# Performance work log

Hardware: AMD Instinct MI355X
Metric: run time of the kernel (lower is better)

## Reference

```python
import jax, jax.numpy as jnp
import numpy as np

N, E, D_IN, HID, OUT, H = 50000, 800000, 64, 128, 128, 8


def _lin(key, fan_in, fan_out, bias=True):
    k1, k2 = jax.random.split(key)
    W = jax.random.normal(k1, (fan_in, fan_out), jnp.float32) / np.sqrt(fan_in)
    if bias:
        b = jax.random.normal(k2, (fan_out,), jnp.float32) * 0.01
        return W, b
    return (W,)


def setup_inputs() -> dict:
    key = jax.random.key(0)
    ks = jax.random.split(key, 40)
    inp = {
        "x": jax.random.normal(ks[0], (N, D_IN), jnp.float32),
        "edge_index": jax.random.randint(ks[1], (2, E), 0, N, jnp.int64),
        "edge_attr": jax.random.normal(ks[2], (E, D_IN), jnp.float32),
    }
    dims = [(D_IN, HID), (HID, HID), (HID, OUT)]  # (in, heads*out_ch) per layer
    ki = 3
    for l, (di, do) in enumerate(dims):
        inp[f"Wq{l}"], inp[f"bq{l}"] = _lin(ks[ki], di, do); ki += 1
        inp[f"Wk{l}"], inp[f"bk{l}"] = _lin(ks[ki], di, do); ki += 1
        inp[f"Wv{l}"], inp[f"bv{l}"] = _lin(ks[ki], di, do); ki += 1
        (inp[f"We{l}"],) = _lin(ks[ki], D_IN, do, bias=False); ki += 1
        inp[f"Ws{l}"], inp[f"bs{l}"] = _lin(ks[ki], di, do); ki += 1
    for l in range(2):
        inp[f"g{l}"] = jnp.ones((HID,), jnp.float32)
        inp[f"be{l}"] = jnp.zeros((HID,), jnp.float32)
    return inp


def _transformer_conv(x, src, dst, edge_attr, Wq, bq, Wk, bk, Wv, bv, We, Ws, bs):
    n = x.shape[0]
    hc = Wq.shape[1]
    c = hc // H
    q = (x @ Wq + bq).reshape(n, H, c)
    k = (x @ Wk + bk).reshape(n, H, c)
    v = (x @ Wv + bv).reshape(n, H, c)
    e = (edge_attr @ We).reshape(-1, H, c)  # [E,H,c]
    ke = k[src] + e                          # edge-wise key + edge proj
    alpha = jnp.einsum("ehc,ehc->eh", q[dst], ke) / jnp.sqrt(jnp.float32(c))
    m = jax.ops.segment_max(alpha, dst, num_segments=n)
    m = jnp.where(jnp.isfinite(m), m, 0.0)
    p = jnp.exp(alpha - m[dst])
    s = jax.ops.segment_sum(p, dst, num_segments=n)
    a = p / (s[dst] + 1e-16)                 # segment softmax over in-edges
    msg = (v[src] + e) * a[..., None]
    out = jax.ops.segment_sum(msg, dst, num_segments=n).reshape(n, hc)
    return out + x @ Ws + bs                 # root/skip connection


def _bn(x, g, b):
    mu = jnp.mean(x, axis=0)
    var = jnp.mean(jnp.square(x - mu), axis=0)
    return g * (x - mu) * jax.lax.rsqrt(var + 1e-5) + b


def reference(x, edge_index, edge_attr,
              Wq0, bq0, Wk0, bk0, Wv0, bv0, We0, Ws0, bs0,
              Wq1, bq1, Wk1, bk1, Wv1, bv1, We1, Ws1, bs1,
              Wq2, bq2, Wk2, bk2, Wv2, bv2, We2, Ws2, bs2,
              g0, be0, g1, be1):
    src, dst = edge_index[0], edge_index[1]
    h = _transformer_conv(x, src, dst, edge_attr, Wq0, bq0, Wk0, bk0, Wv0, bv0, We0, Ws0, bs0)
    h = jax.nn.relu(_bn(h, g0, be0))
    h = _transformer_conv(h, src, dst, edge_attr, Wq1, bq1, Wk1, bk1, Wv1, bv1, We1, Ws1, bs1)
    h = jax.nn.relu(_bn(h, g1, be1))
    h = _transformer_conv(h, src, dst, edge_attr, Wq2, bq2, Wk2, bk2, Wv2, bv2, We2, Ws2, bs2)
    return h, edge_attr
```

## Files before the change

### kernel.cpp

```cpp
#include <hip/hip_runtime.h>
#include <hip/hip_bf16.h>

typedef __attribute__((ext_vector_type(8))) short short8;
typedef __attribute__((ext_vector_type(4))) float f32x4;
typedef unsigned short ushort_t;
typedef __attribute__((ext_vector_type(2))) unsigned short ushort2v;
typedef __attribute__((ext_vector_type(2))) unsigned int uint2v;
typedef __attribute__((ext_vector_type(4))) unsigned int uint4v;

static __device__ __forceinline__ ushort_t f2bf(float x) {
    __hip_bfloat16 h = __float2bfloat16(x);
    return *(ushort_t*)&h;
}
static __device__ __forceinline__ float bflo(unsigned int u) { return __uint_as_float(u << 16); }
static __device__ __forceinline__ float bfhi(unsigned int u) { return __uint_as_float(u & 0xffff0000u); }
static __device__ __forceinline__ float bfu(ushort_t u) { return __uint_as_float((unsigned int)u << 16); }

template <int CTRL>
static __device__ __forceinline__ float dpp_xadd(float x) {
    int y = __builtin_amdgcn_update_dpp(0, __float_as_int(x), CTRL, 0xF, 0xF, true);
    return x + __int_as_float(y);
}


__global__ void hist_kernel(const int* __restrict__ dst, int E, int* __restrict__ hist) {
    int i = blockIdx.x * blockDim.x + threadIdx.x;
    if (i < E) atomicAdd(&hist[dst[i]], 1);
}

__global__ __launch_bounds__(1024) void scan_block_kernel(
    const int* __restrict__ hist, int n, int* __restrict__ row_ptr, int* __restrict__ bsums)
{
    __shared__ int lds[1024];
    int tid = threadIdx.x;
    int i = blockIdx.x * 1024 + tid;
    int vv = (i < n) ? hist[i] : 0;
    lds[tid] = vv;
    __syncthreads();
    for (int off = 1; off < 1024; off <<= 1) {
        int t = (tid >= off) ? lds[tid - off] : 0;
        __syncthreads();
        lds[tid] += t;
        __syncthreads();
    }
    if (i < n) row_ptr[i] = lds[tid] - vv;
    if (tid == 1023) bsums[blockIdx.x] = lds[1023];
}

__global__ void scan_tops_kernel(int* __restrict__ bsums, int nb) {
    if (threadIdx.x == 0 && blockIdx.x == 0) {
        int run = 0;
        for (int i = 0; i < nb; i++) { int t = bsums[i]; bsums[i] = run; run += t; }
    }
}

__global__ __launch_bounds__(256) void scan_add_kernel(
    const int* __restrict__ bsums, int n, int total,
    int* __restrict__ row_ptr, int* __restrict__ cursor)
{
    int i = blockIdx.x * blockDim.x + threadIdx.x;
    if (i < n) {
        int vv = row_ptr[i] + bsums[i >> 10];
        row_ptr[i] = vv;
        cursor[i] = vv;
    }
    if (i == 0) row_ptr[n] = total;
}

__global__ void scatter_kernel(const int* __restrict__ src, const int* __restrict__ dst, int E,
                               int* __restrict__ cursor, int* __restrict__ eid, int* __restrict__ srcs) {
    int i = blockIdx.x * blockDim.x + threadIdx.x;
    if (i < E) {
        int d = dst[i];
        int pos = atomicAdd(&cursor[d], 1);
        eid[pos] = i;
        srcs[pos] = src[i];
    }
}

__global__ __launch_bounds__(256) void permute_ea_kernel(
    const float* __restrict__ edge_attr, const int* __restrict__ eid, int E,
    ushort_t* __restrict__ ea)
{
    int idx = blockIdx.x * blockDim.x + threadIdx.x;
    if (idx >= E * 8) return;
    int j = idx >> 3, seg = idx & 7;
    int rsrc = eid[j];
    const float* s = edge_attr + (size_t)rsrc * 64 + seg * 8;
    float4 f0 = *(const float4*)s;
    float4 f1 = *(const float4*)(s + 4);
    short8 o;
    o[0] = f2bf(f0.x); o[1] = f2bf(f0.y); o[2] = f2bf(f0.z); o[3] = f2bf(f0.w);
    o[4] = f2bf(f1.x); o[5] = f2bf(f1.y); o[6] = f2bf(f1.z); o[7] = f2bf(f1.w);
    *(short8*)(ea + (size_t)j * 64 + seg * 8) = o;
}

__global__ __launch_bounds__(256) void pack_Wnode_kernel(
    const float* __restrict__ Wq, const float* __restrict__ Wk,
    const float* __restrict__ Wv, const float* __restrict__ Ws,
    int DI, ushort_t* __restrict__ dst)
{
    int NKF = DI >> 5;
    int total = DI * 512;
    int idx = blockIdx.x * blockDim.x + threadIdx.x;
    if (idx >= total) return;
    int j = idx & 7;
    int lane = (idx >> 3) & 63;
    int rest = idx >> 9;
    int kf = rest % NKF;
    int t = rest / NKF;
    int kdim = kf * 32 + (lane >> 4) * 8 + j;
    int ncol = t * 16 + (lane & 15);
    const float* W = (ncol < 128) ? Wq : (ncol < 256) ? Wk : (ncol < 384) ? Wv : Ws;
    dst[idx] = f2bf(W[kdim * 128 + (ncol & 127)]);
}

__global__ __launch_bounds__(256) void pack_bias_kernel(
    const float* __restrict__ bq, const float* __restrict__ bk,
    const float* __restrict__ bv, const float* __restrict__ bs,
    float* __restrict__ dst)
{
    int i = threadIdx.x + blockIdx.x * blockDim.x;
    if (i >= 512) return;
    const float* b = (i < 128) ? bq : (i < 256) ? bk : (i < 384) ? bv : bs;
    dst[i] = b[i & 127];
}

__global__ __launch_bounds__(256) void pack_We_kernel(
    const float* __restrict__ We0, const float* __restrict__ We1,
    const float* __restrict__ We2, ushort_t* __restrict__ Bpack)
{
    int idx = blockIdx.x * blockDim.x + threadIdx.x;
    if (idx >= 3 * 8192) return;
    int j = idx & 7;
    int lane = (idx >> 3) & 63;
    int kk = (idx >> 9) & 1;
    int t = (idx >> 10) & 7;
    int layer = idx >> 13;
    const float* We = (layer == 0) ? We0 : (layer == 1) ? We1 : We2;
    int kdim = kk * 32 + (lane >> 4) * 8 + j;
    int ncol = t * 16 + (lane & 15);
    Bpack[idx] = f2bf(We[kdim * 128 + ncol]);
}

template <int DI, bool BN>
__global__ __launch_bounds__(256) void node_gemm_mfma_kernel(
    const float* __restrict__ hin, int N,
    const ushort_t* __restrict__ Bpack, const float* __restrict__ biasc,
    const float* __restrict__ scale, const float* __restrict__ shift,
    float* __restrict__ qout, unsigned int* __restrict__ kvout,
    float* __restrict__ skipout)
{
    constexpr int NKF = DI / 32;
    __shared__ float ctile[64][132];
    __shared__ ushort_t ctileK[64][136];
    int wave = threadIdx.x >> 6;
    int lane = threadIdx.x & 63;
    int tid = threadIdx.x;
    int base = blockIdx.x * 64;
    int m0 = base + wave * 16;

    int mrow = min(m0 + (lane & 15), N - 1);
    const float* arow = hin + (size_t)mrow * DI;
    int koff = (lane >> 4) * 8;

    short8 a[NKF];
#pragma unroll
    for (int kf = 0; kf < NKF; kf++) {
        float4 fa = *(const float4*)(arow + kf * 32 + koff);
        float4 fb = *(const float4*)(arow + kf * 32 + koff + 4);
        if constexpr (BN) {
            int c0 = kf * 32 + koff;
            float4 sa = *(const float4*)(scale + c0);
            float4 sb = *(const float4*)(scale + c0 + 4);
            float4 ha = *(const float4*)(shift + c0);
            float4 hb = *(const float4*)(shift + c0 + 4);
            fa.x = fmaxf(fa.x * sa.x + ha.x, 0.f);
            fa.y = fmaxf(fa.y * sa.y + ha.y, 0.f);
            fa.z = fmaxf(fa.z * sa.z + ha.z, 0.f);
            fa.w = fmaxf(fa.w * sa.w + ha.w, 0.f);
            fb.x = fmaxf(fb.x * sb.x + hb.x, 0.f);
            fb.y = fmaxf(fb.y * sb.y + hb.y, 0.f);
            fb.z = fmaxf(fb.z * sb.z + hb.z, 0.f);
            fb.w = fmaxf(fb.w * sb.w + hb.w, 0.f);
        }
        short8 t;
        t[0] = f2bf(fa.x); t[1] = f2bf(fa.y); t[2] = f2bf(fa.z); t[3] = f2bf(fa.w);
        t[4] = f2bf(fb.x); t[5] = f2bf(fb.y); t[6] = f2bf(fb.z); t[7] = f2bf(fb.w);
        a[kf] = t;
    }

    const short8* Bp = (const short8*)Bpack;
    f32x4 acc[32];
#pragma unroll
    for (int t = 0; t < 32; t++) acc[t] = (f32x4){0.f, 0.f, 0.f, 0.f};
#pragma unroll
    for (int t = 0; t < 32; t++) {
#pragma unroll
        for (int kf = 0; kf < NKF; kf++)
            acc[t] = __builtin_amdgcn_mfma_f32_16x16x32_bf16(a[kf], Bp[(t * NKF + kf) * 64 + lane], acc[t], 0, 0, 0);
    }

    int crow = (lane >> 4) * 4;
    int ccol = lane & 15;

#pragma unroll
    for (int t8 = 0; t8 < 8; t8++) {
        float bb = biasc[t8 * 16 + ccol];
#pragma unroll
        for (int r = 0; r < 4; r++)
            ctile[wave * 16 + crow + r][t8 * 16 + ccol] = acc[t8][r] + bb;
    }
    __syncthreads();
#pragma unroll
    for (int it = 0; it < 8; it++) {
        int idx4 = it * 256 + tid;
        int row = idx4 >> 5;
        int c4 = idx4 & 31;
        int gr = base + row;
        if (gr < N)
            *(float4*)(qout + (size_t)gr * 128 + c4 * 4) = *(const float4*)&ctile[row][c4 * 4];
    }
    __syncthreads();

#pragma unroll
    for (int t8 = 0; t8 < 8; t8++) {
        float bb = biasc[128 + t8 * 16 + ccol];
#pragma unroll
        for (int r = 0; r < 4; r++)
            ctileK[wave * 16 + crow + r][t8 * 16 + ccol] = f2bf(acc[8 + t8][r] + bb);
    }
#pragma unroll
    for (int t8 = 0; t8 < 8; t8++) {
        float bb = biasc[256 + t8 * 16 + ccol];
#pragma unroll
        for (int r = 0; r < 4; r++)
            ctile[wave * 16 + crow + r][t8 * 16 + ccol] = acc[16 + t8][r] + bb;
    }
    __syncthreads();
#pragma unroll
    for (int it = 0; it < 4; it++) {
        int idx8 = it * 256 + tid;
        int row = idx8 >> 4;
        int c8 = idx8 & 15;
        int gr = base + row;
        if (gr < N) {
            const float* vs = &ctile[row][c8 * 8];
            uint4v o0, o1;
#pragma unroll
            for (int i = 0; i < 4; i++) {
                ushort2v kp2 = *(const ushort2v*)&ctileK[row][c8 * 8 + 2 * i];
                unsigned int kp = (unsigned int)kp2[0] | ((unsigned int)kp2[1] << 16);
                unsigned int vp = (unsigned int)f2bf(vs[2 * i]) | ((unsigned int)f2bf(vs[2 * i + 1]) << 16);
                if (i < 2) { o0[2 * i] = kp; o0[2 * i + 1] = vp; }
                else       { o1[2 * (i - 2)] = kp; o1[2 * (i - 2) + 1] = vp; }
            }
            unsigned int* dp = kvout + (size_t)gr * 128 + c8 * 8;
            *(uint4v*)dp = o0;
            *(uint4v*)(dp + 4) = o1;
        }
    }
    __syncthreads();

#pragma unroll
    for (int t8 = 0; t8 < 8; t8++) {
        float bb = biasc[384 + t8 * 16 + ccol];
#pragma unroll
        for (int r = 0; r < 4; r++)
            ctile[wave * 16 + crow + r][t8 * 16 + ccol] = acc[24 + t8][r] + bb;
    }
    __syncthreads();
#pragma unroll
    for (int it = 0; it < 8; it++) {
        int idx4 = it * 256 + tid;
        int row = idx4 >> 5;
        int c4 = idx4 & 31;
        int gr = base + row;
        if (gr < N)
            *(float4*)(skipout + (size_t)gr * 128 + c4 * 4) = *(const float4*)&ctile[row][c4 * 4];
    }
}

#define PROCESS8(B)                                                              \
    {                                                                            \
        ushort2v eev[8];                                                         \
        float p[8];                                                              \
        _Pragma("unroll")                                                        \
        for (int u = 0; u < 8; u++)                                              \
            eev[u] = *(const ushort2v*)&elds[wave][(B) * 8 + u][2 * lane];       \
        _Pragma("unroll")                                                        \
        for (int u = 0; u < 8; u++) {                                            \
            uint2v kvp = kvr[(B) * 8 + u];                                       \
            p[u] = qq.x * (bflo(kvp[0]) + bfu(eev[u][0]))                        \
                 + qq.y * (bfhi(kvp[0]) + bfu(eev[u][1]));                       \
        }                                                                        \
        _Pragma("unroll")                                                        \
        for (int u = 0; u < 8; u++) {                                            \
            p[u] = dpp_xadd<0xB1>(p[u]);                                         \
            p[u] = dpp_xadd<0x4E>(p[u]);                                         \
            p[u] = dpp_xadd<0x141>(p[u]);       \
        }                                                                        \
        _Pragma("unroll")                                                        \
        for (int u = 0; u < 8; u++) {                                            \
            float wv = __expf(p[u] * 0.25f);                                     \
            if (c0 + (B) * 8 + u >= je) wv = 0.f;                                \
            uint2v kvp = kvr[(B) * 8 + u];                                       \
            acc0 += wv * (bflo(kvp[1]) + bfu(eev[u][0]));                        \
            acc1 += wv * (bfhi(kvp[1]) + bfu(eev[u][1]));                        \
            sw += wv;                                                            \
        }                                                                        \
    }

__global__ __launch_bounds__(256) void agg_fused_kernel(
    const int* __restrict__ row_ptr, const int* __restrict__ srcs,
    const float* __restrict__ q, const unsigned int* __restrict__ kvbuf,
    const ushort_t* __restrict__ ea, const ushort_t* __restrict__ BpackWe,
    float* __restrict__ hout, int N)
{
    __shared__ ushort_t elds[4][16][136];
    int tid = threadIdx.x;
    int wave = tid >> 6, lane = tid & 63;
    int n = blockIdx.x * 4 + wave;
    if (n >= N) return;

    const short8* BpG = (const short8*)BpackWe;
    short8 bq[16];
#pragma unroll
    for (int i = 0; i < 16; i++) bq[i] = BpG[i * 64 + lane];

    const float2* q2 = (const float2*)q;
    float2* h2 = (float2*)hout;

    int ch = lane & 15, kg = lane >> 4;
    float2 qq = q2[(size_t)n * 64 + lane];
    float2 sk = h2[(size_t)n * 64 + lane];
    float acc0 = 0.f, acc1 = 0.f, sw = 0.f;
    int jb = row_ptr[n], je = row_ptr[n + 1];

    short8 a0 = {}, a1 = {};
    int sv = 0;
    if (jb < je) {
        int j0 = min(jb + ch, je - 1);
        sv = srcs[j0];
        const ushort_t* row0 = ea + (size_t)j0 * 64;
        a0 = *(const short8*)(row0 + kg * 8);
        a1 = *(const short8*)(row0 + 32 + kg * 8);
    }

    for (int c0 = jb; c0 < je; c0 += 16) {
        uint2v kvr[16];
#pragma unroll
        for (int u = 0; u < 16; u++) {
            int su = __builtin_amdgcn_readlane(sv, u);
            kvr[u] = *(const uint2v*)(kvbuf + (size_t)su * 128 + 2 * lane);
        }

#pragma unroll
        for (int t = 0; t < 8; t++) {
            f32x4 z = (f32x4){0.f, 0.f, 0.f, 0.f};
            z = __builtin_amdgcn_mfma_f32_16x16x32_bf16(a0, bq[t * 2 + 0], z, 0, 0, 0);
            z = __builtin_amdgcn_mfma_f32_16x16x32_bf16(a1, bq[t * 2 + 1], z, 0, 0, 0);
#pragma unroll
            for (int r = 0; r < 4; r++)
                elds[wave][kg * 4 + r][t * 16 + ch] = f2bf(z[r]);
        }

        int cn = c0 + 16;
        short8 na0 = a0, na1 = a1;
        int nsv = sv;
        if (cn < je) {
            int jn = min(cn + ch, je - 1);
            nsv = srcs[jn];
            const ushort_t* nrow = ea + (size_t)jn * 64;
            na0 = *(const short8*)(nrow + kg * 8);
            na1 = *(const short8*)(nrow + 32 + kg * 8);
        }

        asm volatile("" ::: "memory");

        PROCESS8(0)
        if (c0 + 8 < je) PROCESS8(1)

        a0 = na0; a1 = na1; sv = nsv;
    }
    float inv = 1.0f / (sw + 1e-16f);
    float2 o;
    o.x = acc0 * inv + sk.x;
    o.y = acc1 * inv + sk.y;
    h2[(size_t)n * 64 + lane] = o;
}

__global__ __launch_bounds__(128) void bn_stats_kernel(const float* __restrict__ h, int N,
                                                       float* __restrict__ sums) {
    int f = threadIdx.x;
    float s = 0.f, s2 = 0.f;
    for (int n = blockIdx.x; n < N; n += gridDim.x) {
        float x = h[(size_t)n * 128 + f];
        s += x;
        s2 += x * x;
    }
    atomicAdd(&sums[f], s);
    atomicAdd(&sums[128 + f], s2);
}

__global__ __launch_bounds__(128) void bn_finalize_kernel(
    const float* __restrict__ sums, const float* __restrict__ g,
    const float* __restrict__ be, int N,
    float* __restrict__ scale, float* __restrict__ shift)
{
    int f = threadIdx.x;
    float invN = 1.0f / (float)N;
    float mu = sums[f] * invN;
    float var = sums[128 + f] * invN - mu * mu;
    float sc = g[f] * rsqrtf(var + 1e-5f);
    scale[f] = sc;
    shift[f] = be[f] - mu * sc;
}

extern "C" void kernel_launch(void* const* d_in, const int* in_sizes, int n_in,
                              void* d_out, int out_size, void* d_ws, size_t ws_size,
                              hipStream_t stream)
{
    const float* x = (const float*)d_in[0];
    const int* edge_index = (const int*)d_in[1];
    const float* edge_attr = (const float*)d_in[2];
    int N = in_sizes[0] / 64;
    int E = in_sizes[1] / 2;
    const int* src = edge_index;
    const int* dst = edge_index + E;

    const float* W[3][9];
    for (int l = 0; l < 3; l++)
        for (int i = 0; i < 9; i++) W[l][i] = (const float*)d_in[3 + l * 9 + i];
    const float* g0 = (const float*)d_in[30];
    const float* be0 = (const float*)d_in[31];
    const float* g1 = (const float*)d_in[32];
    const float* be1 = (const float*)d_in[33];

    char* p = (char*)d_ws;
    auto alloc = [&](size_t bytes) -> char* {
        char* r = p;
        p += (bytes + 255) & ~(size_t)255;
        return r;
    };
    float* q = (float*)alloc((size_t)N * 128 * 4);
    unsigned int* kvbuf = (unsigned int*)alloc((size_t)N * 512);
    float* B = (float*)alloc((size_t)N * 128 * 4);
    ushort_t* ea = (ushort_t*)alloc((size_t)E * 64 * 2);
    int* row_ptr = (int*)alloc((size_t)(N + 1) * 4);
    int* cursor = (int*)alloc((size_t)N * 4);
    int* histb = (int*)alloc((size_t)N * 4);
    int* eid = (int*)alloc((size_t)E * 4);
    int* srcs = (int*)alloc((size_t)E * 4);
    int* bsums = (int*)alloc(64 * 4);
    float* sums = (float*)alloc(512 * 4);
    float* bnp = (float*)alloc(512 * 4);
    ushort_t* BpackE = (ushort_t*)alloc((size_t)3 * 8192 * 2);
    ushort_t* BpackN = (ushort_t*)alloc((size_t)3 * 65536 * 2);
    float* biasc = (float*)alloc((size_t)3 * 512 * 4);

    int nb = (N + 1023) / 1024;

    hipMemsetAsync(histb, 0, (size_t)N * 4, stream);
    hipMemsetAsync(sums, 0, 512 * 4, stream);
    hist_kernel<<<(E + 255) / 256, 256, 0, stream>>>(dst, E, histb);
    scan_block_kernel<<<nb, 1024, 0, stream>>>(histb, N, row_ptr, bsums);
    scan_tops_kernel<<<1, 64, 0, stream>>>(bsums, nb);
    scan_add_kernel<<<(N + 255) / 256, 256, 0, stream>>>(bsums, N, E, row_ptr, cursor);
    scatter_kernel<<<(E + 255) / 256, 256, 0, stream>>>(src, dst, E, cursor, eid, srcs);
    permute_ea_kernel<<<(E * 8 + 255) / 256, 256, 0, stream>>>(edge_attr, eid, E, ea);

    pack_We_kernel<<<(3 * 8192 + 255) / 256, 256, 0, stream>>>(W[0][6], W[1][6], W[2][6], BpackE);
    for (int l = 0; l < 3; l++) {
        int DI = (l == 0) ? 64 : 128;
        pack_Wnode_kernel<<<(DI * 512 + 255) / 256, 256, 0, stream>>>(
            W[l][0], W[l][2], W[l][4], W[l][7], DI, BpackN + (size_t)l * 65536);
        pack_bias_kernel<<<2, 256, 0, stream>>>(W[l][1], W[l][3], W[l][5], W[l][8],
                                                biasc + (size_t)l * 512);
    }

    for (int l = 0; l < 3; l++) {
        float* skipbuf = (l == 2) ? (float*)d_out : B;
        if (l == 0)
            node_gemm_mfma_kernel<64, false><<<(N + 63) / 64, 256, 0, stream>>>(
                x, N, BpackN, biasc, nullptr, nullptr, q, kvbuf, skipbuf);
        else
            node_gemm_mfma_kernel<128, true><<<(N + 63) / 64, 256, 0, stream>>>(
                B, N, BpackN + (size_t)l * 65536, biasc + (size_t)l * 512,
                bnp + (size_t)(l - 1) * 256, bnp + (size_t)(l - 1) * 256 + 128,
                q, kvbuf, skipbuf);
        agg_fused_kernel<<<(N + 3) / 4, 256, 0, stream>>>(
            row_ptr, srcs, q, kvbuf, ea, BpackE + (size_t)l * 8192, skipbuf, N);
        if (l < 2) {
            bn_stats_kernel<<<512, 128, 0, stream>>>(skipbuf, N, sums + (size_t)l * 256);
            const float* gg = (l == 0) ? g0 : g1;
            const float* bb = (l == 0) ? be0 : be1;
            bn_finalize_kernel<<<1, 128, 0, stream>>>(
                sums + (size_t)l * 256, gg, bb, N,
                bnp + (size_t)l * 256, bnp + (size_t)l * 256 + 128);
        }
    }

    hipMemcpyAsync((float*)d_out + (size_t)N * 128, edge_attr, (size_t)E * 64 * 4,
                   hipMemcpyDeviceToDevice, stream);
}
```

Before: 751.1 us.

## Fuse edge_attr passthrough copy with bf16 permute, merge pack kernels, trim softmax masking

The edge_attr passthrough copy now happens inside the permute kernel. That kernel reads edge_attr once in order, writes the fp32 output copy, and scatters the bf16 version to its CSR position through an inverse index, which removes the separate 205MB device copy. The three weight and bias pack kernels are merged into one launch. In the aggregation loop, the 1/sqrt(c) scale is folded into q once, and full 16-edge chunks skip the per-edge bounds mask. The cost is scattered bf16 writes in place of scattered fp32 reads.

```diff
diff --git a/kernel.cpp b/kernel.cpp
--- a/kernel.cpp
+++ b/kernel.cpp
@@ -68,79 +68,71 @@
 }
 
 __global__ void scatter_kernel(const int* __restrict__ src, const int* __restrict__ dst, int E,
-                               int* __restrict__ cursor, int* __restrict__ eid, int* __restrict__ srcs) {
+                               int* __restrict__ cursor, int* __restrict__ inv, int* __restrict__ srcs) {
     int i = blockIdx.x * blockDim.x + threadIdx.x;
     if (i < E) {
         int d = dst[i];
         int pos = atomicAdd(&cursor[d], 1);
-        eid[pos] = i;
+        inv[i] = pos;
         srcs[pos] = src[i];
     }
 }
 
-__global__ __launch_bounds__(256) void permute_ea_kernel(
-    const float* __restrict__ edge_attr, const int* __restrict__ eid, int E,
-    ushort_t* __restrict__ ea)
+__global__ __launch_bounds__(256) void copy_permute_kernel(
+    const float* __restrict__ edge_attr, const int* __restrict__ inv, int E,
+    float* __restrict__ out_pass, ushort_t* __restrict__ ea)
 {
     int idx = blockIdx.x * blockDim.x + threadIdx.x;
     if (idx >= E * 8) return;
-    int j = idx >> 3, seg = idx & 7;
-    int rsrc = eid[j];
-    const float* s = edge_attr + (size_t)rsrc * 64 + seg * 8;
+    int i = idx >> 3, seg = idx & 7;
+    const float* s = edge_attr + (size_t)i * 64 + seg * 8;
     float4 f0 = *(const float4*)s;
     float4 f1 = *(const float4*)(s + 4);
+    float* d = out_pass + (size_t)i * 64 + seg * 8;
+    *(float4*)d = f0;
+    *(float4*)(d + 4) = f1;
     short8 o;
     o[0] = f2bf(f0.x); o[1] = f2bf(f0.y); o[2] = f2bf(f0.z); o[3] = f2bf(f0.w);
     o[4] = f2bf(f1.x); o[5] = f2bf(f1.y); o[6] = f2bf(f1.z); o[7] = f2bf(f1.w);
-    *(short8*)(ea + (size_t)j * 64 + seg * 8) = o;
-}
-
-__global__ __launch_bounds__(256) void pack_Wnode_kernel(
-    const float* __restrict__ Wq, const float* __restrict__ Wk,
-    const float* __restrict__ Wv, const float* __restrict__ Ws,
-    int DI, ushort_t* __restrict__ dst)
-{
-    int NKF = DI >> 5;
-    int total = DI * 512;
+    int pos = inv[i];
+    *(short8*)(ea + (size_t)pos * 64 + seg * 8) = o;
+}
+
+struct PackArgs {
+    const float* We[3];
+    const float* Wn[3][4];
+    const float* bb[3][4];
+};
+
+__global__ __launch_bounds__(256) void pack_all_kernel(
+    PackArgs pa, ushort_t* __restrict__ BpackE, ushort_t* __restrict__ BpackN,
+    float* __restrict__ biasc)
+{
     int idx = blockIdx.x * blockDim.x + threadIdx.x;
-    if (idx >= total) return;
-    int j = idx & 7;
-    int lane = (idx >> 3) & 63;
-    int rest = idx >> 9;
-    int kf = rest % NKF;
-    int t = rest / NKF;
-    int kdim = kf * 32 + (lane >> 4) * 8 + j;
-    int ncol = t * 16 + (lane & 15);
-    const float* W = (ncol < 128) ? Wq : (ncol < 256) ? Wk : (ncol < 384) ? Wv : Ws;
-    dst[idx] = f2bf(W[kdim * 128 + (ncol & 127)]);
-}
-
-__global__ __launch_bounds__(256) void pack_bias_kernel(
-    const float* __restrict__ bq, const float* __restrict__ bk,
-    const float* __restrict__ bv, const float* __restrict__ bs,
-    float* __restrict__ dst)
-{
-    int i = threadIdx.x + blockIdx.x * blockDim.x;
-    if (i >= 512) return;
-    const float* b = (i < 128) ? bq : (i < 256) ? bk : (i < 384) ? bv : bs;
-    dst[i] = b[i & 127];
-}
-
-__global__ __launch_bounds__(256) void pack_We_kernel(
-    const float* __restrict__ We0, const float* __restrict__ We1,
-    const float* __restrict__ We2, ushort_t* __restrict__ Bpack)
-{
-    int idx = blockIdx.x * blockDim.x + threadIdx.x;
-    if (idx >= 3 * 8192) return;
-    int j = idx & 7;
-    int lane = (idx >> 3) & 63;
-    int kk = (idx >> 9) & 1;
-    int t = (idx >> 10) & 7;
-    int layer = idx >> 13;
-    const float* We = (layer == 0) ? We0 : (layer == 1) ? We1 : We2;
-    int kdim = kk * 32 + (lane >> 4) * 8 + j;
-    int ncol = t * 16 + (lane & 15);
-    Bpack[idx] = f2bf(We[kdim * 128 + ncol]);
+    if (idx < 24576) {
+        int j = idx & 7, lane = (idx >> 3) & 63, kk = (idx >> 9) & 1,
+            t = (idx >> 10) & 7, layer = idx >> 13;
+        int kdim = kk * 32 + (lane >> 4) * 8 + j;
+        int ncol = t * 16 + (lane & 15);
+        BpackE[idx] = f2bf(pa.We[layer][kdim * 128 + ncol]);
+    } else if (idx < 188416) {
+        int local = idx - 24576;
+        int layer, DI;
+        if (local < 32768) { layer = 0; DI = 64; }
+        else if (local < 98304) { layer = 1; DI = 128; local -= 32768; }
+        else { layer = 2; DI = 128; local -= 98304; }
+        int NKF = DI >> 5;
+        int j = local & 7, lane = (local >> 3) & 63;
+        int rest = local >> 9;
+        int kf = rest % NKF, t = rest / NKF;
+        int kdim = kf * 32 + (lane >> 4) * 8 + j;
+        int ncol = t * 16 + (lane & 15);
+        BpackN[layer * 65536 + local] = f2bf(pa.Wn[layer][ncol >> 7][kdim * 128 + (ncol & 127)]);
+    } else if (idx < 189952) {
+        int local = idx - 188416;
+        int layer = local >> 9, i = local & 511;
+        biasc[layer * 512 + i] = pa.bb[layer][i >> 7][i & 127];
+    }
 }
 
 template <int DI, bool BN>
@@ -281,7 +273,7 @@
     }
 }
 
-#define PROCESS8(B)                                                              \
+#define PROCESS8(B, MASKED)                                                      \
     {                                                                            \
         ushort2v eev[8];                                                         \
         float p[8];                                                              \
@@ -302,8 +294,8 @@
         }                                                                        \
         _Pragma("unroll")                                                        \
         for (int u = 0; u < 8; u++) {                                            \
-            float wv = __expf(p[u] * 0.25f);                                     \
-            if (c0 + (B) * 8 + u >= je) wv = 0.f;                                \
+            float wv = __expf(p[u]);                                             \
+            if ((MASKED) && (c0 + (B) * 8 + u >= je)) wv = 0.f;                  \
             uint2v kvp = kvr[(B) * 8 + u];                                       \
             acc0 += wv * (bflo(kvp[1]) + bfu(eev[u][0]));                        \
             acc1 += wv * (bfhi(kvp[1]) + bfu(eev[u][1]));                        \
@@ -333,6 +325,7 @@
 
     int ch = lane & 15, kg = lane >> 4;
     float2 qq = q2[(size_t)n * 64 + lane];
+    qq.x *= 0.25f; qq.y *= 0.25f;
     float2 sk = h2[(size_t)n * 64 + lane];
     float acc0 = 0.f, acc1 = 0.f, sw = 0.f;
     int jb = row_ptr[n], je = row_ptr[n + 1];
@@ -378,8 +371,13 @@
 
         asm volatile("" ::: "memory");
 
-        PROCESS8(0)
-        if (c0 + 8 < je) PROCESS8(1)
+        if (je - c0 >= 16) {
+            PROCESS8(0, 0)
+            PROCESS8(1, 0)
+        } else {
+            PROCESS8(0, 1)
+            if (c0 + 8 < je) PROCESS8(1, 1)
+        }
 
         a0 = na0; a1 = na1; sv = nsv;
     }
@@ -450,7 +448,7 @@
     int* row_ptr = (int*)alloc((size_t)(N + 1) * 4);
     int* cursor = (int*)alloc((size_t)N * 4);
     int* histb = (int*)alloc((size_t)N * 4);
-    int* eid = (int*)alloc((size_t)E * 4);
+    int* inv = (int*)alloc((size_t)E * 4);
     int* srcs = (int*)alloc((size_t)E * 4);
     int* bsums = (int*)alloc(64 * 4);
     float* sums = (float*)alloc(512 * 4);
@@ -467,16 +465,20 @@
     scan_block_kernel<<<nb, 1024, 0, stream>>>(histb, N, row_ptr, bsums);
     scan_tops_kernel<<<1, 64, 0, stream>>>(bsums, nb);
     scan_add_kernel<<<(N + 255) / 256, 256, 0, stream>>>(bsums, N, E, row_ptr, cursor);
-    scatter_kernel<<<(E + 255) / 256, 256, 0, stream>>>(src, dst, E, cursor, eid, srcs);
-    permute_ea_kernel<<<(E * 8 + 255) / 256, 256, 0, stream>>>(edge_attr, eid, E, ea);
-
-    pack_We_kernel<<<(3 * 8192 + 255) / 256, 256, 0, stream>>>(W[0][6], W[1][6], W[2][6], BpackE);
-    for (int l = 0; l < 3; l++) {
-        int DI = (l == 0) ? 64 : 128;
-        pack_Wnode_kernel<<<(DI * 512 + 255) / 256, 256, 0, stream>>>(
-            W[l][0], W[l][2], W[l][4], W[l][7], DI, BpackN + (size_t)l * 65536);
-        pack_bias_kernel<<<2, 256, 0, stream>>>(W[l][1], W[l][3], W[l][5], W[l][8],
-                                                biasc + (size_t)l * 512);
+    scatter_kernel<<<(E + 255) / 256, 256, 0, stream>>>(src, dst, E, cursor, inv, srcs);
+    copy_permute_kernel<<<(E * 8 + 255) / 256, 256, 0, stream>>>(
+        edge_attr, inv, E, (float*)d_out + (size_t)N * 128, ea);
+
+    {
+        PackArgs pa;
+        for (int l = 0; l < 3; l++) {
+            pa.We[l] = W[l][6];
+            pa.Wn[l][0] = W[l][0]; pa.Wn[l][1] = W[l][2];
+            pa.Wn[l][2] = W[l][4]; pa.Wn[l][3] = W[l][7];
+            pa.bb[l][0] = W[l][1]; pa.bb[l][1] = W[l][3];
+            pa.bb[l][2] = W[l][5]; pa.bb[l][3] = W[l][8];
+        }
+        pack_all_kernel<<<(189952 + 255) / 256, 256, 0, stream>>>(pa, BpackE, BpackN, biasc);
     }
 
     for (int l = 0; l < 3; l++) {
@@ -500,7 +502,4 @@
                 bnp + (size_t)l * 256, bnp + (size_t)l * 256 + 128);
         }
     }
-
-    hipMemcpyAsync((float*)d_out + (size_t)N * 128, edge_attr, (size_t)E * 64 * 4,
-                   hipMemcpyDeviceToDevice, stream);
-}
+}
```

Result: slower. 771.9 us (+2.8%).
